# Kernel optimization log

Measured on AMD Instinct MI355X. Metric: run time of the kernel, lower is better.

Reference implementation:

```python
import jax, jax.numpy as jnp
import numpy as np

B, S, D, P, R, NL = 16, 2048, 1024, 8192, 16, 64  # docs, seq, d_model, pairs, n_relations, n_label_pairs
MAX_SPAN = 32


def setup_inputs() -> dict:
    key = jax.random.key(0)
    ks = jax.random.split(key, 8)
    tokvecs = jax.random.normal(ks[0], (B, S, D), dtype=jnp.float32)
    batch_idx = jax.random.randint(ks[1], (P,), 0, B, dtype=jnp.int32)
    e1s = jax.random.randint(ks[2], (P,), 0, S - MAX_SPAN, dtype=jnp.int32)
    e1e = e1s + 1 + jax.random.randint(ks[3], (P,), 0, MAX_SPAN - 1, dtype=jnp.int32)
    e2s = jax.random.randint(ks[4], (P,), 0, S - MAX_SPAN, dtype=jnp.int32)
    e2e = e2s + 1 + jax.random.randint(ks[5], (P,), 0, MAX_SPAN - 1, dtype=jnp.int32)
    rel_idx = jax.random.randint(ks[6], (P,), 0, NL, dtype=jnp.int32)
    # multi-hot relationship-inclusion table (0/1 entries, as built in __init__)
    rel_table = (jax.random.uniform(ks[7], (NL, R)) < 0.25).astype(jnp.float32)
    return {
        "tokvecs": tokvecs,
        "batch_idx": batch_idx,
        "ent1_start": e1s,
        "ent1_end": e1e,
        "ent2_start": e2s,
        "ent2_end": e2e,
        "rel_idx": rel_idx,
        "rel_table": rel_table,
    }


def _span_mean(cs, b, s, e):
    # cs: [B, S+1, D] exclusive prefix sums; span mean = (cs[e] - cs[s]) / (e - s)
    seg = cs[b, e] - cs[b, s]                      # [P, D]
    return seg / (e - s)[:, None].astype(seg.dtype)


def reference(tokvecs, batch_idx, ent1_start, ent1_end, ent2_start, ent2_end, rel_idx, rel_table):
    Bn, Sn, Dn = tokvecs.shape
    # exclusive prefix sum along sequence -> O(1) mean per span instead of ragged gathers
    cs = jnp.concatenate(
        [jnp.zeros((Bn, 1, Dn), tokvecs.dtype), jnp.cumsum(tokvecs, axis=1)], axis=1
    )                                               # [B, S+1, D]
    m1 = _span_mean(cs, batch_idx, ent1_start, ent1_end)   # [P, D]
    m2 = _span_mean(cs, batch_idx, ent2_start, ent2_end)   # [P, D]
    rel = rel_table[rel_idx]                                # [P, R]
    return jnp.concatenate([m1, m2, rel], axis=-1)          # [P, 2D + R]
```

## Files before the change

### kernel.cpp

```cpp
#include <hip/hip_runtime.h>

#define S_LEN      2048
#define D_DIM      1024
#define R_DIM      16
#define OUT_STRIDE 2064
#define NBUCK      8192
#define BPT        8
#define GROUP      4

__global__ __launch_bounds__(1024) void sort_jobs(
    const int* __restrict__ bidx, const int* __restrict__ e1s,
    const int* __restrict__ e2s, int* __restrict__ sorted, int njobs)
{
    __shared__ int hist[NBUCK];
    __shared__ int part[1024];
    const int t = threadIdx.x;

#pragma unroll
    for (int i = 0; i < BPT; ++i) hist[t * BPT + i] = 0;
    __syncthreads();

    for (int j = t; j < njobs; j += 1024) {
        const int p = j >> 1;
        const int s = (j & 1) ? e2s[p] : e1s[p];
        atomicAdd(&hist[(bidx[p] * S_LEN + s) >> 2], 1);
    }
    __syncthreads();

    int v[BPT];
    int sum = 0;
#pragma unroll
    for (int i = 0; i < BPT; ++i) { v[i] = hist[t * BPT + i]; sum += v[i]; }
    part[t] = sum;
    __syncthreads();
    for (int off = 1; off < 1024; off <<= 1) {
        int x = (t >= off) ? part[t - off] : 0;
        __syncthreads();
        part[t] += x;
        __syncthreads();
    }
    int run = (t == 0) ? 0 : part[t - 1];
#pragma unroll
    for (int i = 0; i < BPT; ++i) { int c = v[i]; hist[t * BPT + i] = run; run += c; }
    __syncthreads();

    for (int j = t; j < njobs; j += 1024) {
        const int p = j >> 1;
        const int s = (j & 1) ? e2s[p] : e1s[p];
        const int pos = atomicAdd(&hist[(bidx[p] * S_LEN + s) >> 2], 1);
        sorted[pos] = j;
    }
}

__global__ __launch_bounds__(128) void gather_g4(
    const float* __restrict__ tok,
    const int*   __restrict__ sorted,
    const int*   __restrict__ bidx,
    const int*   __restrict__ e1s, const int* __restrict__ e1e,
    const int*   __restrict__ e2s, const int* __restrict__ e2e,
    const int*   __restrict__ ridx,
    const float* __restrict__ rtab,
    float*       __restrict__ out)
{
    const int blk = blockIdx.x;
    const int w  = (blk & 7) * (gridDim.x >> 3) + (blk >> 3);
    const int g  = w >> 1;
    const int ch = w & 1;
    const int t  = threadIdx.x;

    int   jp[GROUP], jh[GROUP], js[GROUP], je[GROUP];
    float jw[GROUP];
    int mins = 0x7fffffff, maxe = 0;
#pragma unroll
    for (int i = 0; i < GROUP; ++i) {
        const int id = __builtin_amdgcn_readfirstlane(sorted[g * GROUP + i]);
        const int p  = id >> 1;
        const int h  = id & 1;
        const int b  = __builtin_amdgcn_readfirstlane(bidx[p]);
        const int s  = __builtin_amdgcn_readfirstlane(h ? e2s[p] : e1s[p]);
        const int e  = __builtin_amdgcn_readfirstlane(h ? e2e[p] : e1e[p]);
        jp[i] = p; jh[i] = h;
        js[i] = b * S_LEN + s;
        je[i] = b * S_LEN + e;
        jw[i] = 1.0f / (float)(e - s);
        mins  = min(mins, js[i]);
        maxe  = max(maxe, je[i]);
    }

    float4 acc[GROUP];
#pragma unroll
    for (int i = 0; i < GROUP; ++i) acc[i] = make_float4(0.f, 0.f, 0.f, 0.f);

    const float4* base = reinterpret_cast<const float4*>(tok) +
                         (size_t)mins * (D_DIM / 4) + ch * 128 + t;
    const int nrows = maxe - mins;
    const int rmax  = nrows - 1;
    const int niter = (nrows + 3) >> 2;

    float4 cur[4];
#pragma unroll
    for (int k = 0; k < 4; ++k)
        cur[k] = base[(size_t)min(k, rmax) * (D_DIM / 4)];

    for (int it = 0; it < niter; ++it) {
        const int r0 = it * 4;
        float4 nxt[4];
#pragma unroll
        for (int k = 0; k < 4; ++k)
            nxt[k] = base[(size_t)min(r0 + 4 + k, rmax) * (D_DIM / 4)];

        const int gr = mins + r0;
#pragma unroll
        for (int i = 0; i < GROUP; ++i) {
            const float w0 = (gr + 0 >= js[i] && gr + 0 < je[i]) ? jw[i] : 0.f;
            const float w1 = (gr + 1 >= js[i] && gr + 1 < je[i]) ? jw[i] : 0.f;
            const float w2 = (gr + 2 >= js[i] && gr + 2 < je[i]) ? jw[i] : 0.f;
            const float w3 = (gr + 3 >= js[i] && gr + 3 < je[i]) ? jw[i] : 0.f;
            acc[i].x += cur[0].x * w0 + cur[1].x * w1 + cur[2].x * w2 + cur[3].x * w3;
            acc[i].y += cur[0].y * w0 + cur[1].y * w1 + cur[2].y * w2 + cur[3].y * w3;
            acc[i].z += cur[0].z * w0 + cur[1].z * w1 + cur[2].z * w2 + cur[3].z * w3;
            acc[i].w += cur[0].w * w0 + cur[1].w * w1 + cur[2].w * w2 + cur[3].w * w3;
        }
#pragma unroll
        for (int k = 0; k < 4; ++k) cur[k] = nxt[k];
    }

#pragma unroll
    for (int i = 0; i < GROUP; ++i) {
        float* dst = out + (size_t)jp[i] * OUT_STRIDE + jh[i] * D_DIM +
                     ch * 512 + t * 4;
        *reinterpret_cast<float4*>(dst) = acc[i];
        if (ch == 0 && jh[i] == 0 && t < 4) {
            const float4 rv = *reinterpret_cast<const float4*>(
                rtab + ridx[jp[i]] * R_DIM + t * 4);
            *reinterpret_cast<float4*>(
                out + (size_t)jp[i] * OUT_STRIDE + 2 * D_DIM + t * 4) = rv;
        }
    }
}

extern "C" void kernel_launch(void* const* d_in, const int* in_sizes, int n_in,
                              void* d_out, int out_size, void* d_ws, size_t ws_size,
                              hipStream_t stream) {
    const float* tok  = (const float*)d_in[0];
    const int*   bidx = (const int*)d_in[1];
    const int*   e1s  = (const int*)d_in[2];
    const int*   e1e  = (const int*)d_in[3];
    const int*   e2s  = (const int*)d_in[4];
    const int*   e2e  = (const int*)d_in[5];
    const int*   ridx = (const int*)d_in[6];
    const float* rtab = (const float*)d_in[7];
    float*       out  = (float*)d_out;

    const int P     = in_sizes[1];
    const int njobs = 2 * P;

    int* sorted = (int*)d_ws;

    sort_jobs<<<1, 1024, 0, stream>>>(bidx, e1s, e2s, sorted, njobs);

    const int nblocks = (njobs / GROUP) * 2;
    gather_g4<<<nblocks, 128, 0, stream>>>(
        tok, sorted, bidx, e1s, e1e, e2s, e2e, ridx, rtab, out);
}
```

Measured before the change: 268.1 us.

## Stage token rows into LDS via async global_load_lds with double buffering

The gather kernel now uses 256-thread blocks that each cover a full 1024-wide row for a group of 4 jobs, where before two 128-thread blocks each covered half a row. Token rows are copied straight from global memory into a double-buffered shared-memory tile using the global_load_lds builtin, four rows per stage, one wave per row. This is meant to cut register pressure and overlap loads with the FMA work. It adds a block-wide barrier per stage and halves the block count, which may reduce latency hiding.

Result: no change. 268.2 us (+0.1%).

```diff
diff --git a/kernel.cpp b/kernel.cpp
--- a/kernel.cpp
+++ b/kernel.cpp
@@ -7,6 +7,7 @@
 #define NBUCK      8192
 #define BPT        8
 #define GROUP      4
+#define NR         4
 
 __global__ __launch_bounds__(1024) void sort_jobs(
     const int* __restrict__ bidx, const int* __restrict__ e1s,
@@ -52,7 +53,13 @@
     }
 }
 
-__global__ __launch_bounds__(128) void gather_g4(
+__device__ __forceinline__ void load16_lds(const float* g, float* l) {
+    __builtin_amdgcn_global_load_lds(
+        (const __attribute__((address_space(1))) void*)g,
+        (__attribute__((address_space(3))) void*)l, 16, 0, 0);
+}
+
+__global__ __launch_bounds__(256) void gather_lds(
     const float* __restrict__ tok,
     const int*   __restrict__ sorted,
     const int*   __restrict__ bidx,
@@ -62,11 +69,13 @@
     const float* __restrict__ rtab,
     float*       __restrict__ out)
 {
+    __shared__ float buf[2][NR * D_DIM];
+
     const int blk = blockIdx.x;
-    const int w  = (blk & 7) * (gridDim.x >> 3) + (blk >> 3);
-    const int g  = w >> 1;
-    const int ch = w & 1;
+    const int g  = (blk & 7) * (gridDim.x >> 3) + (blk >> 3);
     const int t  = threadIdx.x;
+    const int wv = t >> 6;
+    const int ln = t & 63;
 
     int   jp[GROUP], jh[GROUP], js[GROUP], je[GROUP];
     float jw[GROUP];
@@ -87,50 +96,54 @@
         maxe  = max(maxe, je[i]);
     }
 
+    const int nrows = maxe - mins;
+    const int rmaxg = maxe - 1;
+    const int niter = (nrows + NR - 1) / NR;
+
+    auto stage = [&](int bi, int c) {
+        const int grow = min(mins + c * NR + wv, rmaxg);
+        const float* src = tok + (size_t)grow * D_DIM + ln * 4;
+        float* dst = &buf[bi][wv * D_DIM];
+#pragma unroll
+        for (int q = 0; q < 4; ++q)
+            load16_lds(src + q * 256, dst + q * 256);
+    };
+
+    stage(0, 0);
+
     float4 acc[GROUP];
 #pragma unroll
     for (int i = 0; i < GROUP; ++i) acc[i] = make_float4(0.f, 0.f, 0.f, 0.f);
 
-    const float4* base = reinterpret_cast<const float4*>(tok) +
-                         (size_t)mins * (D_DIM / 4) + ch * 128 + t;
-    const int nrows = maxe - mins;
-    const int rmax  = nrows - 1;
-    const int niter = (nrows + 3) >> 2;
+    __syncthreads();
 
-    float4 cur[4];
+    for (int c = 0; c < niter; ++c) {
+        if (c + 1 < niter) stage((c + 1) & 1, c + 1);
+
+        const int cb  = c & 1;
+        const int gr0 = mins + c * NR;
 #pragma unroll
-    for (int k = 0; k < 4; ++k)
-        cur[k] = base[(size_t)min(k, rmax) * (D_DIM / 4)];
-
-    for (int it = 0; it < niter; ++it) {
-        const int r0 = it * 4;
-        float4 nxt[4];
+        for (int r = 0; r < NR; ++r) {
+            const float4 v = *reinterpret_cast<const float4*>(
+                &buf[cb][r * D_DIM + t * 4]);
+            const int gr = gr0 + r;
 #pragma unroll
-        for (int k = 0; k < 4; ++k)
-            nxt[k] = base[(size_t)min(r0 + 4 + k, rmax) * (D_DIM / 4)];
-
-        const int gr = mins + r0;
-#pragma unroll
-        for (int i = 0; i < GROUP; ++i) {
-            const float w0 = (gr + 0 >= js[i] && gr + 0 < je[i]) ? jw[i] : 0.f;
-            const float w1 = (gr + 1 >= js[i] && gr + 1 < je[i]) ? jw[i] : 0.f;
-            const float w2 = (gr + 2 >= js[i] && gr + 2 < je[i]) ? jw[i] : 0.f;
-            const float w3 = (gr + 3 >= js[i] && gr + 3 < je[i]) ? jw[i] : 0.f;
-            acc[i].x += cur[0].x * w0 + cur[1].x * w1 + cur[2].x * w2 + cur[3].x * w3;
-            acc[i].y += cur[0].y * w0 + cur[1].y * w1 + cur[2].y * w2 + cur[3].y * w3;
-            acc[i].z += cur[0].z * w0 + cur[1].z * w1 + cur[2].z * w2 + cur[3].z * w3;
-            acc[i].w += cur[0].w * w0 + cur[1].w * w1 + cur[2].w * w2 + cur[3].w * w3;
+            for (int i = 0; i < GROUP; ++i) {
+                const float w = (gr >= js[i] && gr < je[i]) ? jw[i] : 0.f;
+                acc[i].x += v.x * w;
+                acc[i].y += v.y * w;
+                acc[i].z += v.z * w;
+                acc[i].w += v.w * w;
+            }
         }
-#pragma unroll
-        for (int k = 0; k < 4; ++k) cur[k] = nxt[k];
+        __syncthreads();
     }
 
 #pragma unroll
     for (int i = 0; i < GROUP; ++i) {
-        float* dst = out + (size_t)jp[i] * OUT_STRIDE + jh[i] * D_DIM +
-                     ch * 512 + t * 4;
+        float* dst = out + (size_t)jp[i] * OUT_STRIDE + jh[i] * D_DIM + t * 4;
         *reinterpret_cast<float4*>(dst) = acc[i];
-        if (ch == 0 && jh[i] == 0 && t < 4) {
+        if (jh[i] == 0 && t < 4) {
             const float4 rv = *reinterpret_cast<const float4*>(
                 rtab + ridx[jp[i]] * R_DIM + t * 4);
             *reinterpret_cast<float4*>(
@@ -159,7 +172,7 @@
 
     sort_jobs<<<1, 1024, 0, stream>>>(bidx, e1s, e2s, sorted, njobs);
 
-    const int nblocks = (njobs / GROUP) * 2;
-    gather_g4<<<nblocks, 128, 0, stream>>>(
+    const int nblocks = njobs / GROUP;
+    gather_lds<<<nblocks, 256, 0, stream>>>(
         tok, sorted, bidx, e1s, e1e, e2s, e2e, ridx, rtab, out);
 }
```

## Group 16 sorted spans per wave and split feature dim into quarters

Applied to the files above, without the earlier changes.

Each block now handles 16 sorted span jobs instead of 4, using a single 64-lane wave that covers a quarter of the feature dimension. Neighbouring spans share overlapping token rows, so one read of each row can feed more outputs. The explicit next-row prefetch buffer is dropped, the span-bounds test becomes a single unsigned compare, and job ids are reloaded at store time to save registers. In exchange the row window per group widens, so each wave scans rows that fall outside many of its spans and does more wasted multiply-adds. With 16 accumulators per lane, register pressure and occupancy may also suffer.

New measurement: 468.8 us. 74.9% more time.

```diff
diff --git a/kernel.cpp b/kernel.cpp
--- a/kernel.cpp
+++ b/kernel.cpp
@@ -6,7 +6,8 @@
 #define OUT_STRIDE 2064
 #define NBUCK      8192
 #define BPT        8
-#define GROUP      4
+#define G          16
+#define QW         256
 
 __global__ __launch_bounds__(1024) void sort_jobs(
     const int* __restrict__ bidx, const int* __restrict__ e1s,
@@ -52,7 +53,7 @@
     }
 }
 
-__global__ __launch_bounds__(128) void gather_g4(
+__global__ __launch_bounds__(64, 4) void gather_g16q(
     const float* __restrict__ tok,
     const int*   __restrict__ sorted,
     const int*   __restrict__ bidx,
@@ -64,77 +65,72 @@
 {
     const int blk = blockIdx.x;
     const int w  = (blk & 7) * (gridDim.x >> 3) + (blk >> 3);
-    const int g  = w >> 1;
-    const int ch = w & 1;
-    const int t  = threadIdx.x;
+    const int g  = w >> 2;
+    const int ch = w & 3;
+    const int ln = threadIdx.x;
 
-    int   jp[GROUP], jh[GROUP], js[GROUP], je[GROUP];
-    float jw[GROUP];
+    int   js[G], jlen[G];
+    float jw[G];
     int mins = 0x7fffffff, maxe = 0;
 #pragma unroll
-    for (int i = 0; i < GROUP; ++i) {
-        const int id = __builtin_amdgcn_readfirstlane(sorted[g * GROUP + i]);
+    for (int i = 0; i < G; ++i) {
+        const int id = __builtin_amdgcn_readfirstlane(sorted[g * G + i]);
         const int p  = id >> 1;
         const int h  = id & 1;
         const int b  = __builtin_amdgcn_readfirstlane(bidx[p]);
         const int s  = __builtin_amdgcn_readfirstlane(h ? e2s[p] : e1s[p]);
         const int e  = __builtin_amdgcn_readfirstlane(h ? e2e[p] : e1e[p]);
-        jp[i] = p; jh[i] = h;
-        js[i] = b * S_LEN + s;
-        je[i] = b * S_LEN + e;
-        jw[i] = 1.0f / (float)(e - s);
-        mins  = min(mins, js[i]);
-        maxe  = max(maxe, je[i]);
+        js[i]   = b * S_LEN + s;
+        jlen[i] = e - s;
+        jw[i]   = 1.0f / (float)(e - s);
+        mins = min(mins, js[i]);
+        maxe = max(maxe, b * S_LEN + e);
     }
 
-    float4 acc[GROUP];
-#pragma unroll
-    for (int i = 0; i < GROUP; ++i) acc[i] = make_float4(0.f, 0.f, 0.f, 0.f);
-
-    const float4* base = reinterpret_cast<const float4*>(tok) +
-                         (size_t)mins * (D_DIM / 4) + ch * 128 + t;
     const int nrows = maxe - mins;
     const int rmax  = nrows - 1;
     const int niter = (nrows + 3) >> 2;
 
-    float4 cur[4];
+    const float4* base = reinterpret_cast<const float4*>(tok) +
+                         (size_t)mins * (D_DIM / 4) + ch * (QW / 4) + ln;
+
+    float4 acc[G];
 #pragma unroll
-    for (int k = 0; k < 4; ++k)
-        cur[k] = base[(size_t)min(k, rmax) * (D_DIM / 4)];
+    for (int i = 0; i < G; ++i) acc[i] = make_float4(0.f, 0.f, 0.f, 0.f);
 
     for (int it = 0; it < niter; ++it) {
         const int r0 = it * 4;
-        float4 nxt[4];
+        float4 cur[4];
 #pragma unroll
         for (int k = 0; k < 4; ++k)
-            nxt[k] = base[(size_t)min(r0 + 4 + k, rmax) * (D_DIM / 4)];
+            cur[k] = base[(size_t)min(r0 + k, rmax) * (D_DIM / 4)];
 
         const int gr = mins + r0;
 #pragma unroll
-        for (int i = 0; i < GROUP; ++i) {
-            const float w0 = (gr + 0 >= js[i] && gr + 0 < je[i]) ? jw[i] : 0.f;
-            const float w1 = (gr + 1 >= js[i] && gr + 1 < je[i]) ? jw[i] : 0.f;
-            const float w2 = (gr + 2 >= js[i] && gr + 2 < je[i]) ? jw[i] : 0.f;
-            const float w3 = (gr + 3 >= js[i] && gr + 3 < je[i]) ? jw[i] : 0.f;
+        for (int i = 0; i < G; ++i) {
+            const float w0 = ((unsigned)(gr + 0 - js[i]) < (unsigned)jlen[i]) ? jw[i] : 0.f;
+            const float w1 = ((unsigned)(gr + 1 - js[i]) < (unsigned)jlen[i]) ? jw[i] : 0.f;
+            const float w2 = ((unsigned)(gr + 2 - js[i]) < (unsigned)jlen[i]) ? jw[i] : 0.f;
+            const float w3 = ((unsigned)(gr + 3 - js[i]) < (unsigned)jlen[i]) ? jw[i] : 0.f;
             acc[i].x += cur[0].x * w0 + cur[1].x * w1 + cur[2].x * w2 + cur[3].x * w3;
             acc[i].y += cur[0].y * w0 + cur[1].y * w1 + cur[2].y * w2 + cur[3].y * w3;
             acc[i].z += cur[0].z * w0 + cur[1].z * w1 + cur[2].z * w2 + cur[3].z * w3;
             acc[i].w += cur[0].w * w0 + cur[1].w * w1 + cur[2].w * w2 + cur[3].w * w3;
         }
-#pragma unroll
-        for (int k = 0; k < 4; ++k) cur[k] = nxt[k];
     }
 
 #pragma unroll
-    for (int i = 0; i < GROUP; ++i) {
-        float* dst = out + (size_t)jp[i] * OUT_STRIDE + jh[i] * D_DIM +
-                     ch * 512 + t * 4;
+    for (int i = 0; i < G; ++i) {
+        const int id = __builtin_amdgcn_readfirstlane(sorted[g * G + i]);
+        const int p  = id >> 1;
+        const int h  = id & 1;
+        float* dst = out + (size_t)p * OUT_STRIDE + h * D_DIM + ch * QW + ln * 4;
         *reinterpret_cast<float4*>(dst) = acc[i];
-        if (ch == 0 && jh[i] == 0 && t < 4) {
+        if (ch == 0 && h == 0 && ln < 4) {
             const float4 rv = *reinterpret_cast<const float4*>(
-                rtab + ridx[jp[i]] * R_DIM + t * 4);
+                rtab + ridx[p] * R_DIM + ln * 4);
             *reinterpret_cast<float4*>(
-                out + (size_t)jp[i] * OUT_STRIDE + 2 * D_DIM + t * 4) = rv;
+                out + (size_t)p * OUT_STRIDE + 2 * D_DIM + ln * 4) = rv;
         }
     }
 }
@@ -159,7 +155,7 @@
 
     sort_jobs<<<1, 1024, 0, stream>>>(bidx, e1s, e2s, sorted, njobs);
 
-    const int nblocks = (njobs / GROUP) * 2;
-    gather_g4<<<nblocks, 128, 0, stream>>>(
+    const int nblocks = (njobs / G) * 4;
+    gather_g16q<<<nblocks, 64, 0, stream>>>(
         tok, sorted, bidx, e1s, e1e, e2s, e2e, ridx, rtab, out);
 }
```
